# Performance work log

Hardware: AMD Instinct MI355X
Metric: run time of the kernel (lower is better)

The kernel has to match this reference:

```python
import jax, jax.numpy as jnp
import numpy as np

D = 1024
H = 16
HD = D // H
FF = 4096
EPS = 1e-5
B, L = 8, 1024

def setup_inputs() -> dict:
    key = jax.random.key(0)
    ks = jax.random.split(key, 12)
    s = lambda k, shape: jax.random.normal(k, shape, dtype=jnp.float32) * (shape[0] ** -0.5)
    return {
        "x": jax.random.normal(ks[0], (B, L, D), dtype=jnp.float32),
        "attention_mask": jnp.ones((B, L), dtype=jnp.int32),
        "wq": s(ks[1], (D, D)), "bq": jnp.zeros((D,), jnp.float32),
        "wk": s(ks[2], (D, D)), "bk": jnp.zeros((D,), jnp.float32),
        "wv": s(ks[3], (D, D)), "bv": jnp.zeros((D,), jnp.float32),
        "wo": s(ks[4], (D, D)), "bo": jnp.zeros((D,), jnp.float32),
        "ln1_s": jnp.ones((D,), jnp.float32), "ln1_b": jnp.zeros((D,), jnp.float32),
        "ln2_s": jnp.ones((D,), jnp.float32), "ln2_b": jnp.zeros((D,), jnp.float32),
        "w1": s(ks[5], (D, FF)), "b1": jnp.zeros((FF,), jnp.float32),
        "w2": s(ks[6], (FF, D)), "b2": jnp.zeros((D,), jnp.float32),
    }

def _layer_norm(x, scale, bias):
    mu = jnp.mean(x, axis=-1, keepdims=True)
    var = jnp.mean(jnp.square(x - mu), axis=-1, keepdims=True)
    return (x - mu) * jax.lax.rsqrt(var + EPS) * scale + bias

def _quick_gelu(x):
    return x * jax.nn.sigmoid(1.702 * x)

def reference(x, attention_mask, wq, bq, wk, bk, wv, bv, wo, bo,
              ln1_s, ln1_b, ln2_s, ln2_b, w1, b1, w2, b2):
    Bc, Lc, Dc = x.shape
    scale = HD ** -0.5
    # --- attention block (pre-LN) ---
    h = _layer_norm(x, ln1_s, ln1_b)
    to_heads = lambda t: t.reshape(Bc, Lc, H, HD).transpose(0, 2, 1, 3)
    q = to_heads(h @ wq + bq)
    k = to_heads(h @ wk + bk)
    v = to_heads(h @ wv + bv)
    scores = jnp.einsum('bhqd,bhkd->bhqk', q.astype(jnp.float32), k.astype(jnp.float32)) * scale
    fmask = jnp.where(attention_mask[:, None, None, :] > 0, 0.0,
                      jnp.finfo(scores.dtype).min)
    weights = jax.nn.softmax(scores + fmask, axis=-1)
    attn = jnp.einsum('bhqk,bhkd->bhqd', weights, v.astype(jnp.float32))
    attn = attn.transpose(0, 2, 1, 3).reshape(Bc, Lc, Dc).astype(x.dtype)
    x = x + (attn @ wo + bo)
    # --- MLP block (pre-LN) ---
    h = _layer_norm(x, ln2_s, ln2_b)
    h = _quick_gelu(h @ w1 + b1) @ w2 + b2
    return x + h
```

## Files before the change

### kernel.cpp

```cpp
#include <hip/hip_runtime.h>
#include <math.h>

#define D_MODEL 1024
#define N_TOK   8192
#define SEQ_L   1024
#define N_HEAD  16
#define HEAD_D  64
#define FF_DIM  4096

typedef __attribute__((ext_vector_type(8))) short bf16x8;
typedef __attribute__((ext_vector_type(4))) short short4v;
typedef __attribute__((ext_vector_type(2))) int  int2v;
typedef __attribute__((ext_vector_type(4))) float f32x4;

#define MFMA16(a, b, c) __builtin_amdgcn_mfma_f32_16x16x32_bf16((a), (b), (c), 0, 0, 0)

#define GLD16(gp, lp) __builtin_amdgcn_global_load_lds(                      \
    (const __attribute__((address_space(1))) void*)(gp),                     \
    (__attribute__((address_space(3))) void*)(lp), 16, 0, 0)

#if defined(__has_builtin)
#if __has_builtin(__builtin_amdgcn_exp2f)
#define EXP2F(x) __builtin_amdgcn_exp2f(x)
#else
#define EXP2F(x) exp2f(x)
#endif
#else
#define EXP2F(x) exp2f(x)
#endif

__device__ __forceinline__ short f2bf(float f) {
    unsigned u = __float_as_uint(f);
    u += 0x7fffu + ((u >> 16) & 1u);
    return (short)(u >> 16);
}

__device__ __forceinline__ int pack2bf(float a, float b) {
    unsigned ua = __float_as_uint(a) + 0x8000u;
    unsigned ub = __float_as_uint(b) + 0x8000u;
    return __builtin_amdgcn_perm(ub, ua, 0x07060302u);
}

__global__ __launch_bounds__(256) void ln_kernel(const float* __restrict__ x,
                                                 const float* __restrict__ g,
                                                 const float* __restrict__ b,
                                                 short* __restrict__ o)
{
    int t = blockIdx.x;
    const float* xr = x + (size_t)t * D_MODEL;
    short* orow = o + (size_t)t * D_MODEL;
    float vals[4];
    float lsum = 0.f, lsq = 0.f;
#pragma unroll
    for (int i = 0; i < 4; i++) {
        float v = xr[threadIdx.x + i * 256];
        vals[i] = v; lsum += v; lsq += v * v;
    }
#pragma unroll
    for (int off = 32; off > 0; off >>= 1) {
        lsum += __shfl_down(lsum, off);
        lsq  += __shfl_down(lsq,  off);
    }
    __shared__ float red[8];
    int wid = threadIdx.x >> 6, lane = threadIdx.x & 63;
    if (lane == 0) { red[wid] = lsum; red[4 + wid] = lsq; }
    __syncthreads();
    if (threadIdx.x == 0) {
        red[0] = red[0] + red[1] + red[2] + red[3];
        red[4] = red[4] + red[5] + red[6] + red[7];
    }
    __syncthreads();
    float mean = red[0] * (1.f / D_MODEL);
    float var  = red[4] * (1.f / D_MODEL) - mean * mean;
    float inv  = rsqrtf(var + 1e-5f);
#pragma unroll
    for (int i = 0; i < 4; i++) {
        int c = threadIdx.x + i * 256;
        orow[c] = f2bf((vals[i] - mean) * inv * g[c] + b[c]);
    }
}

__global__ __launch_bounds__(256) void mask_kernel(const int* __restrict__ m,
                                                   float* __restrict__ fm)
{
    int i = blockIdx.x * 256 + threadIdx.x;
    fm[i] = (m[i] > 0) ? 0.f : -1e30f;
}

__global__ __launch_bounds__(256) void transpose_cast(const float* __restrict__ src,
                                                      short* __restrict__ dst,
                                                      int R, int C)
{
    __shared__ float t[32][33];
    int r0 = blockIdx.y * 32, c0 = blockIdx.x * 32;
    int tid = threadIdx.x;
#pragma unroll
    for (int i = 0; i < 4; i++) {
        int idx = i * 256 + tid;
        int r = idx >> 5, c = idx & 31;
        t[r][c] = src[(size_t)(r0 + r) * C + c0 + c];
    }
    __syncthreads();
#pragma unroll
    for (int i = 0; i < 4; i++) {
        int idx = i * 256 + tid;
        int rr = idx >> 5, cc = idx & 31;
        dst[(size_t)(c0 + rr) * R + r0 + cc] = f2bf(t[cc][rr]);
    }
}

__global__ __launch_bounds__(256) void gemm_bf16(
    const short* __restrict__ A, int lda,
    const short* __restrict__ Bt, int ldb,
    const float* __restrict__ bias,
    const float* __restrict__ bias2,
    const float* __restrict__ bias3,
    const float* __restrict__ resid,
    float* __restrict__ Cf, short* __restrict__ Cb, short* __restrict__ Cvt,
    int ldc, int K, int act, int qkv)
{
    __shared__ __align__(16) short sA[128 * 32];
    __shared__ __align__(16) short sB[128 * 32];
    const int tid = threadIdx.x;
    const int lane = tid & 63, wave = tid >> 6;
    const int quad = lane >> 4, l15 = lane & 15;
    const int bm = blockIdx.y * 128, bn = blockIdx.x * 128;
    const int wm = (wave >> 1) * 64, wn = (wave & 1) * 64;

    const int ca = tid, cb = tid + 256;
    const int ra = ca >> 2, ka = (ca & 3) << 3;
    const int rb = cb >> 2, kb = (cb & 3) << 3;

    f32x4 acc[4][4];
#pragma unroll
    for (int i = 0; i < 4; i++)
#pragma unroll
        for (int j = 0; j < 4; j++) acc[i][j] = (f32x4){0.f, 0.f, 0.f, 0.f};

    for (int k0 = 0; k0 < K; k0 += 32) {
        __syncthreads();
        GLD16(A  + (size_t)(bm + ra) * lda + k0 + ka, &sA[ca * 8]);
        GLD16(A  + (size_t)(bm + rb) * lda + k0 + kb, &sA[cb * 8]);
        GLD16(Bt + (size_t)(bn + ra) * ldb + k0 + ka, &sB[ca * 8]);
        GLD16(Bt + (size_t)(bn + rb) * ldb + k0 + kb, &sB[cb * 8]);
        __syncthreads();
        bf16x8 af[4], bfr[4];
#pragma unroll
        for (int mt = 0; mt < 4; mt++)
            af[mt] = *(const bf16x8*)&sA[(wm + mt * 16 + l15) * 32 + quad * 8];
#pragma unroll
        for (int nt = 0; nt < 4; nt++)
            bfr[nt] = *(const bf16x8*)&sB[(wn + nt * 16 + l15) * 32 + quad * 8];
#pragma unroll
        for (int mt = 0; mt < 4; mt++)
#pragma unroll
            for (int nt = 0; nt < 4; nt++)
                acc[mt][nt] = MFMA16(af[mt], bfr[nt], acc[mt][nt]);
    }

#pragma unroll
    for (int mt = 0; mt < 4; mt++)
#pragma unroll
        for (int nt = 0; nt < 4; nt++) {
            int row0 = bm + wm + mt * 16 + quad * 4;
            int col  = bn + wn + nt * 16 + l15;
            if (qkv) {
                int seg = col >> 10, cloc = col & 1023;
                const float* bp = (seg == 0) ? bias : (seg == 1) ? bias2 : bias3;
                float bval = bp[cloc];
                if (seg == 2) {
                    int bb = row0 >> 10, l0 = row0 & 1023;
                    size_t page = (size_t)(bb * N_HEAD + (cloc >> 6)) * HEAD_D + (cloc & 63);
                    short4v pk = { f2bf(acc[mt][nt][0] + bval), f2bf(acc[mt][nt][1] + bval),
                                   f2bf(acc[mt][nt][2] + bval), f2bf(acc[mt][nt][3] + bval) };
                    *(short4v*)&Cvt[page * SEQ_L + l0] = pk;
                } else {
                    short* dst = Cb + (size_t)seg * ((size_t)N_TOK * D_MODEL);
#pragma unroll
                    for (int r = 0; r < 4; r++)
                        dst[(size_t)(row0 + r) * D_MODEL + cloc] = f2bf(acc[mt][nt][r] + bval);
                }
            } else {
#pragma unroll
                for (int r = 0; r < 4; r++) {
                    int row = row0 + r;
                    float v = acc[mt][nt][r] + bias[col];
                    if (act) v = v / (1.f + __expf(-1.702f * v));
                    if (resid) v += resid[(size_t)row * ldc + col];
                    if (Cb) Cb[(size_t)row * ldc + col] = f2bf(v);
                    else    Cf[(size_t)row * ldc + col] = v;
                }
            }
        }
}

__global__ __launch_bounds__(256) void attn_kernel(
    const short* __restrict__ Q, const short* __restrict__ Kb,
    const short* __restrict__ Vt, const float* __restrict__ fmask,
    short* __restrict__ O)
{
    __shared__ __align__(16) short sK[8192];
    __shared__ __align__(16) short sV[8192];
    __shared__ __align__(16) short sP[4][16 * 136];
    __shared__ __align__(16) float sAl[4][20];

    const int g = blockIdx.x;
    const int xcd = g & 7, slot = g >> 3;
    const int qt = slot & 15, bhl = slot >> 4;
    const int bh = xcd * 16 + bhl;
    const int b = bh >> 4, h = bh & 15;

    const int tid = threadIdx.x;
    const int wave = tid >> 6, lane = tid & 63;
    const int quad = lane >> 4, l15 = lane & 15;

    const int qbase = b * SEQ_L + qt * 64;
    const short* qp = Q + (size_t)(qbase + wave * 16 + l15) * D_MODEL + h * HEAD_D + quad * 8;
    bf16x8 qf0 = *(const bf16x8*)qp;
    bf16x8 qf1 = *(const bf16x8*)(qp + 32);

    const short* Kbh = Kb + (size_t)b * SEQ_L * D_MODEL + h * HEAD_D;
    const short* Vbh = Vt + (size_t)(b * N_HEAD + h) * HEAD_D * SEQ_L;
    const float* mk  = fmask + b * SEQ_L;

    f32x4 o4[4];
#pragma unroll
    for (int nt = 0; nt < 4; nt++) o4[nt] = (f32x4){0.f, 0.f, 0.f, 0.f};
    float mrow = -1e30f, lrow = 0.f;
    short* pslab = &sP[wave][0];
    const float CSC = 0.125f * 1.4426950408889634f;

    for (int kt = 0; kt < SEQ_L / 128; kt++) {
        __syncthreads();
#pragma unroll
        for (int j = 0; j < 4; j++) {
            int cid = wave * 4 + j;
            int kc = cid >> 1, key0 = (cid & 1) << 6;
            GLD16(Kbh + (size_t)(kt * 128 + key0 + lane) * D_MODEL + kc * 8,
                  &sK[cid * 512]);
            GLD16(Vbh + (size_t)lane * SEQ_L + kt * 128 + cid * 8,
                  &sV[cid * 512]);
        }
        __syncthreads();

        f32x4 mkv[8];
#pragma unroll
        for (int sub = 0; sub < 8; sub++)
            mkv[sub] = *(const f32x4*)&mk[kt * 128 + sub * 16 + quad * 4];

        f32x4 s[8];
#pragma unroll
        for (int sub = 0; sub < 8; sub++) {
            bf16x8 kf0 = *(const bf16x8*)&sK[(quad * 128 + sub * 16 + l15) * 8];
            bf16x8 kf1 = *(const bf16x8*)&sK[((quad + 4) * 128 + sub * 16 + l15) * 8];
            s[sub] = (f32x4){0.f, 0.f, 0.f, 0.f};
            s[sub] = MFMA16(kf0, qf0, s[sub]);
            s[sub] = MFMA16(kf1, qf1, s[sub]);
        }
#pragma unroll
        for (int sub = 0; sub < 8; sub++)
#pragma unroll
            for (int r = 0; r < 4; r++) s[sub][r] = s[sub][r] * CSC + mkv[sub][r];

        f32x4 mx4 = s[0];
#pragma unroll
        for (int sub = 1; sub < 8; sub++)
#pragma unroll
            for (int r = 0; r < 4; r++) mx4[r] = fmaxf(mx4[r], s[sub][r]);
        float pmax = fmaxf(fmaxf(mx4[0], mx4[1]), fmaxf(mx4[2], mx4[3]));
        pmax = fmaxf(pmax, __shfl_xor(pmax, 16));
        pmax = fmaxf(pmax, __shfl_xor(pmax, 32));
        float mnew = fmaxf(mrow, pmax);
        float alpha = EXP2F(mrow - mnew);
        mrow = mnew;
        if (quad == 0) sAl[wave][l15] = alpha;

        float ls = 0.f;
#pragma unroll
        for (int sub = 0; sub < 8; sub++) {
            float p0 = EXP2F(s[sub][0] - mnew);
            float p1 = EXP2F(s[sub][1] - mnew);
            float p2 = EXP2F(s[sub][2] - mnew);
            float p3 = EXP2F(s[sub][3] - mnew);
            ls += (p0 + p1) + (p2 + p3);
            int2v pk = { pack2bf(p0, p1), pack2bf(p2, p3) };
            *(int2v*)&pslab[l15 * 136 + sub * 16 + quad * 4] = pk;
        }
        ls += __shfl_xor(ls, 16);
        ls += __shfl_xor(ls, 32);
        lrow = lrow * alpha + ls;

        f32x4 av = *(const f32x4*)&sAl[wave][quad * 4];
#pragma unroll
        for (int nt = 0; nt < 4; nt++)
#pragma unroll
            for (int r = 0; r < 4; r++) o4[nt][r] *= av[r];

        bf16x8 pf[4];
#pragma unroll
        for (int c = 0; c < 4; c++)
            pf[c] = *(const bf16x8*)&pslab[l15 * 136 + c * 32 + quad * 8];
#pragma unroll
        for (int nt = 0; nt < 4; nt++)
#pragma unroll
            for (int c = 0; c < 4; c++) {
                bf16x8 vfr = *(const bf16x8*)&sV[((c * 4 + quad) * 64 + nt * 16 + l15) * 8];
                o4[nt] = MFMA16(pf[c], vfr, o4[nt]);
            }
    }
    if (quad == 0) sAl[wave][l15] = 1.f / lrow;
    __syncthreads();
    f32x4 iv = *(const f32x4*)&sAl[wave][quad * 4];
#pragma unroll
    for (int nt = 0; nt < 4; nt++)
#pragma unroll
        for (int r = 0; r < 4; r++)
            O[(size_t)(qbase + wave * 16 + quad * 4 + r) * D_MODEL
              + h * HEAD_D + nt * 16 + l15] = f2bf(o4[nt][r] * iv[r]);
}

extern "C" void kernel_launch(void* const* d_in, const int* in_sizes, int n_in,
                              void* d_out, int out_size, void* d_ws, size_t ws_size,
                              hipStream_t stream)
{
    const float* x     = (const float*)d_in[0];
    const int*   amask = (const int*)  d_in[1];
    const float* wq    = (const float*)d_in[2];
    const float* bq    = (const float*)d_in[3];
    const float* wk    = (const float*)d_in[4];
    const float* bk    = (const float*)d_in[5];
    const float* wv    = (const float*)d_in[6];
    const float* bv    = (const float*)d_in[7];
    const float* wo    = (const float*)d_in[8];
    const float* bo    = (const float*)d_in[9];
    const float* ln1s  = (const float*)d_in[10];
    const float* ln1b  = (const float*)d_in[11];
    const float* ln2s  = (const float*)d_in[12];
    const float* ln2b  = (const float*)d_in[13];
    const float* w1    = (const float*)d_in[14];
    const float* b1    = (const float*)d_in[15];
    const float* w2    = (const float*)d_in[16];
    const float* b2    = (const float*)d_in[17];
    float* out = (float*)d_out;

    char* w = (char*)d_ws;
    short* wqkvt = (short*)(w + (size_t)0);
    short* wot   = (short*)(w + ((size_t)6  << 20));
    short* w1t   = (short*)(w + ((size_t)8  << 20));
    short* w2t   = (short*)(w + ((size_t)16 << 20));
    short* hb    = (short*)(w + ((size_t)24 << 20));
    short* qb    = (short*)(w + ((size_t)40 << 20));
    short* kbf   = (short*)(w + ((size_t)56 << 20));
    short* attnb = (short*)(w + ((size_t)72 << 20));
    short* vtb   = (short*)(w + ((size_t)88 << 20));
    short* ffb   = qb;
    float* fmaskb = (float*)(w + ((size_t)24 << 20));

    dim3 blk(256);

    transpose_cast<<<dim3(32, 32),  blk, 0, stream>>>(wq, wqkvt,              1024, 1024);
    transpose_cast<<<dim3(32, 32),  blk, 0, stream>>>(wk, wqkvt + 1024 * 1024, 1024, 1024);
    transpose_cast<<<dim3(32, 32),  blk, 0, stream>>>(wv, wqkvt + 2048 * 1024, 1024, 1024);
    transpose_cast<<<dim3(32, 32),  blk, 0, stream>>>(wo, wot, 1024, 1024);
    transpose_cast<<<dim3(128, 32), blk, 0, stream>>>(w1, w1t, 1024, 4096);
    transpose_cast<<<dim3(32, 128), blk, 0, stream>>>(w2, w2t, 4096, 1024);

    ln_kernel<<<N_TOK, blk, 0, stream>>>(x, ln1s, ln1b, hb);

    gemm_bf16<<<dim3(3 * D_MODEL / 128, N_TOK / 128), blk, 0, stream>>>(
        hb, 1024, wqkvt, 1024, bq, bk, bv, nullptr,
        nullptr, qb, vtb, 1024, 1024, 0, 1);

    mask_kernel<<<dim3(8 * SEQ_L / 256), blk, 0, stream>>>(amask, fmaskb);

    attn_kernel<<<dim3(2048), blk, 0, stream>>>(qb, kbf, vtb, fmaskb, attnb);

    gemm_bf16<<<dim3(D_MODEL / 128, N_TOK / 128), blk, 0, stream>>>(
        attnb, 1024, wot, 1024, bo, nullptr, nullptr, x,
        out, nullptr, nullptr, 1024, 1024, 0, 0);

    ln_kernel<<<N_TOK, blk, 0, stream>>>(out, ln2s, ln2b, hb);

    gemm_bf16<<<dim3(FF_DIM / 128, N_TOK / 128), blk, 0, stream>>>(
        hb, 1024, w1t, 1024, b1, nullptr, nullptr, nullptr,
        nullptr, ffb, nullptr, 4096, 1024, 1, 0);
    gemm_bf16<<<dim3(D_MODEL / 128, N_TOK / 128), blk, 0, stream>>>(
        ffb, 4096, w2t, 4096, b2, nullptr, nullptr, out,
        out, nullptr, nullptr, 1024, 4096, 0, 0);
}
```

Before: 652.6 us.

## Double GEMM K-tile to 64 with k-chunk-major LDS layout; merge weight transposes

The GEMM now stages 64-wide K slices per iteration instead of 32, which halves the number of barrier pairs per output tile. The shared-memory layout becomes k-chunk-major (8-element chunks by 128 rows), so each wave's global_load_lds writes a contiguous 512-element run. It also aims to change LDS read bank patterns. Separately, the six weight transpose/cast launches are merged into one prep kernel, cutting launch overhead. LDS use doubles to 32KB per block, which may reduce occupancy.

```diff
diff --git a/kernel.cpp b/kernel.cpp
--- a/kernel.cpp
+++ b/kernel.cpp
@@ -87,12 +87,27 @@
     fm[i] = (m[i] > 0) ? 0.f : -1e30f;
 }
 
-__global__ __launch_bounds__(256) void transpose_cast(const float* __restrict__ src,
-                                                      short* __restrict__ dst,
-                                                      int R, int C)
-{
+__global__ __launch_bounds__(256) void prep_kernel(
+    const float* __restrict__ wq, const float* __restrict__ wk,
+    const float* __restrict__ wv, const float* __restrict__ wo,
+    const float* __restrict__ w1, const float* __restrict__ w2,
+    short* __restrict__ wqkvt, short* __restrict__ wot,
+    short* __restrict__ w1t,  short* __restrict__ w2t)
+{
+    int id = blockIdx.x;
+    const float* src; short* dst; int R, C, tloc, csh;
+    if (id < 4096) {
+        int wsel = id >> 10; tloc = id & 1023; R = 1024; C = 1024; csh = 5;
+        src = (wsel == 0) ? wq : (wsel == 1) ? wk : (wsel == 2) ? wv : wo;
+        dst = (wsel == 3) ? wot : (wqkvt + (size_t)wsel * 1024 * 1024);
+    } else if (id < 8192) {
+        tloc = id - 4096; R = 1024; C = 4096; csh = 7; src = w1; dst = w1t;
+    } else {
+        tloc = id - 8192; R = 4096; C = 1024; csh = 5; src = w2; dst = w2t;
+    }
+    int ty = tloc >> csh, tx = tloc & ((1 << csh) - 1);
+    int r0 = ty * 32, c0 = tx * 32;
     __shared__ float t[32][33];
-    int r0 = blockIdx.y * 32, c0 = blockIdx.x * 32;
     int tid = threadIdx.x;
 #pragma unroll
     for (int i = 0; i < 4; i++) {
@@ -119,43 +134,47 @@
     float* __restrict__ Cf, short* __restrict__ Cb, short* __restrict__ Cvt,
     int ldc, int K, int act, int qkv)
 {
-    __shared__ __align__(16) short sA[128 * 32];
-    __shared__ __align__(16) short sB[128 * 32];
+    __shared__ __align__(16) short sA[128 * 64];
+    __shared__ __align__(16) short sB[128 * 64];
     const int tid = threadIdx.x;
     const int lane = tid & 63, wave = tid >> 6;
     const int quad = lane >> 4, l15 = lane & 15;
     const int bm = blockIdx.y * 128, bn = blockIdx.x * 128;
     const int wm = (wave >> 1) * 64, wn = (wave & 1) * 64;
 
-    const int ca = tid, cb = tid + 256;
-    const int ra = ca >> 2, ka = (ca & 3) << 3;
-    const int rb = cb >> 2, kb = (cb & 3) << 3;
-
     f32x4 acc[4][4];
 #pragma unroll
     for (int i = 0; i < 4; i++)
 #pragma unroll
         for (int j = 0; j < 4; j++) acc[i][j] = (f32x4){0.f, 0.f, 0.f, 0.f};
 
-    for (int k0 = 0; k0 < K; k0 += 32) {
+    for (int k0 = 0; k0 < K; k0 += 64) {
         __syncthreads();
-        GLD16(A  + (size_t)(bm + ra) * lda + k0 + ka, &sA[ca * 8]);
-        GLD16(A  + (size_t)(bm + rb) * lda + k0 + kb, &sA[cb * 8]);
-        GLD16(Bt + (size_t)(bn + ra) * ldb + k0 + ka, &sB[ca * 8]);
-        GLD16(Bt + (size_t)(bn + rb) * ldb + k0 + kb, &sB[cb * 8]);
+#pragma unroll
+        for (int j = 0; j < 4; j++) {
+            int cid = wave * 4 + j;
+            int kc = cid >> 1, rb0 = (cid & 1) << 6;
+            GLD16(A  + (size_t)(bm + rb0 + lane) * lda + k0 + kc * 8,
+                  &sA[cid * 512]);
+            GLD16(Bt + (size_t)(bn + rb0 + lane) * ldb + k0 + kc * 8,
+                  &sB[cid * 512]);
+        }
         __syncthreads();
-        bf16x8 af[4], bfr[4];
-#pragma unroll
-        for (int mt = 0; mt < 4; mt++)
-            af[mt] = *(const bf16x8*)&sA[(wm + mt * 16 + l15) * 32 + quad * 8];
-#pragma unroll
-        for (int nt = 0; nt < 4; nt++)
-            bfr[nt] = *(const bf16x8*)&sB[(wn + nt * 16 + l15) * 32 + quad * 8];
-#pragma unroll
-        for (int mt = 0; mt < 4; mt++)
+#pragma unroll
+        for (int ko = 0; ko < 2; ko++) {
+            bf16x8 af[4], bfr[4];
+#pragma unroll
+            for (int mt = 0; mt < 4; mt++)
+                af[mt] = *(const bf16x8*)&sA[((ko * 4 + quad) * 128 + wm + mt * 16 + l15) * 8];
 #pragma unroll
             for (int nt = 0; nt < 4; nt++)
-                acc[mt][nt] = MFMA16(af[mt], bfr[nt], acc[mt][nt]);
+                bfr[nt] = *(const bf16x8*)&sB[((ko * 4 + quad) * 128 + wn + nt * 16 + l15) * 8];
+#pragma unroll
+            for (int mt = 0; mt < 4; mt++)
+#pragma unroll
+                for (int nt = 0; nt < 4; nt++)
+                    acc[mt][nt] = MFMA16(af[mt], bfr[nt], acc[mt][nt]);
+        }
     }
 
 #pragma unroll
@@ -358,12 +377,8 @@
 
     dim3 blk(256);
 
-    transpose_cast<<<dim3(32, 32),  blk, 0, stream>>>(wq, wqkvt,              1024, 1024);
-    transpose_cast<<<dim3(32, 32),  blk, 0, stream>>>(wk, wqkvt + 1024 * 1024, 1024, 1024);
-    transpose_cast<<<dim3(32, 32),  blk, 0, stream>>>(wv, wqkvt + 2048 * 1024, 1024, 1024);
-    transpose_cast<<<dim3(32, 32),  blk, 0, stream>>>(wo, wot, 1024, 1024);
-    transpose_cast<<<dim3(128, 32), blk, 0, stream>>>(w1, w1t, 1024, 4096);
-    transpose_cast<<<dim3(32, 128), blk, 0, stream>>>(w2, w2t, 4096, 1024);
+    prep_kernel<<<dim3(12288), blk, 0, stream>>>(wq, wk, wv, wo, w1, w2,
+                                                 wqkvt, wot, w1t, w2t);
 
     ln_kernel<<<N_TOK, blk, 0, stream>>>(x, ln1s, ln1b, hb);
 
```

Result: slower. 750.3 us (+15.0%).
